# Kernel tuning notes

Hardware: AMD Instinct MI355X
Metric: run time of the kernel (lower is better)

## Reference

```python
import jax, jax.numpy as jnp
import numpy as np

N = 50000      # graph nodes
E = 800000     # edges
R = 8          # relations
D = 128        # entity_dim == relation_dim == n_hidden
L = 2          # gnn layers
NE = 150000    # entity vocab
NEG_SLOPE = 0.01


def setup_inputs() -> dict:
    key = jax.random.key(0)
    ks = jax.random.split(key, 9)
    return {
        "node_ids": jax.random.randint(ks[0], (N,), 0, NE),
        "relation_ids": jax.random.randint(ks[1], (E,), 0, R),
        "src": jax.random.randint(ks[2], (E,), 0, N),
        "dst": jax.random.randint(ks[3], (E,), 0, N),
        "entity_table": jax.random.normal(ks[4], (NE, D), dtype=jnp.float32) * 0.1,
        "relation_table": jax.random.normal(ks[5], (R, D), dtype=jnp.float32) * 0.1,
        "relation_W": jax.random.normal(ks[6], (R, D, D), dtype=jnp.float32) * 0.1,
        "res_fc_W": jax.random.normal(ks[7], (L, D, D), dtype=jnp.float32) * 0.1,
        "res_fc2_W": jax.random.normal(ks[8], (L, D, D), dtype=jnp.float32) * 0.1,
    }


def _kgat_layer(h, efeat, rel, src, dst, relation_W, W1, W2):
    # project every node by every relation weight: (N, R, D)
    proj = jnp.einsum('nd,rde->nre', h, relation_W)
    t_r = proj[src, rel]            # (E, D)  W_r h_src
    h_r = proj[dst, rel]            # (E, D)  W_r h_dst
    # att = (W_r h_t)^T tanh(W_r h_dst + e_r)
    att = jnp.sum(t_r * jnp.tanh(h_r + efeat), axis=1)  # (E,)
    # edge softmax over incoming edges of each dst node
    m = jax.ops.segment_max(att, dst, num_segments=N)
    ex = jnp.exp(att - m[dst])
    s = jax.ops.segment_sum(ex, dst, num_segments=N)
    a = ex / s[dst]                 # (E,)
    # message = a * h_src, scatter-sum to dst
    h_nb = jax.ops.segment_sum(h[src] * a[:, None], dst, num_segments=N)  # (N, D)
    out = (jax.nn.leaky_relu((h + h_nb) @ W1.T, NEG_SLOPE)
           + jax.nn.leaky_relu((h * h_nb) @ W2.T, NEG_SLOPE))
    return h_nb, out


def reference(node_ids, relation_ids, src, dst, entity_table, relation_table,
              relation_W, res_fc_W, res_fc2_W):
    h = entity_table[node_ids]           # (N, D)
    efeat = relation_table[relation_ids]  # (E, D)
    cache = [h]
    for i in range(L):
        h, out = _kgat_layer(h, efeat, relation_ids, src, dst,
                             relation_W, res_fc_W[i], res_fc2_W[i])
        cache.append(out)
    return jnp.concatenate(cache, axis=1)  # (N, D*(L+1))
```

## Files before the change

### kernel.cpp

```cpp
#include <hip/hip_runtime.h>
#include <math.h>

#define DDIM 128
#define RREL 8

typedef _Float16 f16;
typedef __attribute__((ext_vector_type(2))) _Float16 h2;
typedef __attribute__((ext_vector_type(8))) _Float16 f16x8;
typedef __attribute__((ext_vector_type(4))) float f32x4;

static __device__ __forceinline__ unsigned short f2h(float f) {
    union { _Float16 h; unsigned short s; } c; c.h = (_Float16)f; return c.s;
}
static __device__ __forceinline__ h2 u2h(unsigned u) {
    union { unsigned u; h2 h; } c; c.u = u; return c.h;
}
static __device__ __forceinline__ unsigned h2u(h2 h) {
    union { unsigned u; h2 h; } c; c.h = h; return c.u;
}
static __device__ __forceinline__ float lrelu(float x) {
    return x > 0.0f ? x : 0.01f * x;
}
static __device__ __forceinline__ float tanh_fast(float x) {
    return 1.0f - 2.0f / (__expf(2.0f * x) + 1.0f);
}

__global__ __launch_bounds__(256) void prep_weights(const float* __restrict__ relW,
                                                    const float* __restrict__ fcW,
                                                    const float* __restrict__ fc2W,
                                                    unsigned short* __restrict__ Wt,
                                                    unsigned short* __restrict__ Wb1,
                                                    unsigned short* __restrict__ Wb2) {
    int i = blockIdx.x * 256 + threadIdx.x;
    const int NT = RREL * DDIM * DDIM;
    const int NF = 2 * DDIM * DDIM;
    if (i < NT) {
        int r = i >> 14;
        int d = (i >> 7) & 127;
        int e = i & 127;
        Wt[(r << 14) + (e << 7) + d] = f2h(relW[i]);
    } else if (i < NT + NF) {
        int j = i - NT;
        Wb1[j] = f2h(fcW[j]);
    } else if (i < NT + 2 * NF) {
        int j = i - NT - NF;
        Wb2[j] = f2h(fc2W[j]);
    }
}

__global__ __launch_bounds__(256) void gather_h0(const int* __restrict__ node_ids,
                                                 const float* __restrict__ etab,
                                                 unsigned short* __restrict__ hb0,
                                                 float* __restrict__ out, int N) {
    int i = blockIdx.x * 256 + threadIdx.x;
    if (i >= N * 32) return;
    int n = i >> 5;
    int c4 = (i & 31) * 4;
    float4 v = *(const float4*)(etab + (size_t)node_ids[n] * DDIM + c4);
    *(float4*)(out + (size_t)n * 384 + c4) = v;
    unsigned lo = (unsigned)f2h(v.x) | ((unsigned)f2h(v.y) << 16);
    unsigned hi = (unsigned)f2h(v.z) | ((unsigned)f2h(v.w) << 16);
    *(uint2*)(hb0 + (size_t)n * DDIM + c4) = make_uint2(lo, hi);
}

__global__ __launch_bounds__(256) void hist_k(const int* __restrict__ dst,
                                              int* __restrict__ counts, int E) {
    int i = blockIdx.x * 256 + threadIdx.x;
    if (i < E) atomicAdd(counts + dst[i], 1);
}

__global__ __launch_bounds__(256) void scan_a(const int* __restrict__ counts,
                                              int* __restrict__ tmp,
                                              int* __restrict__ part, int N) {
    __shared__ int sh[256];
    int i = blockIdx.x * 256 + threadIdx.x;
    int v = (i < N) ? counts[i] : 0;
    sh[threadIdx.x] = v;
    __syncthreads();
    #pragma unroll
    for (int o = 1; o < 256; o <<= 1) {
        int t = (threadIdx.x >= o) ? sh[threadIdx.x - o] : 0;
        __syncthreads();
        sh[threadIdx.x] += t;
        __syncthreads();
    }
    if (i < N) tmp[i] = sh[threadIdx.x];
    if (threadIdx.x == 255) part[blockIdx.x] = sh[255];
}

__global__ __launch_bounds__(256) void scan_b(int* __restrict__ part, int nb) {
    __shared__ int sh[256];
    int v = (threadIdx.x < nb) ? part[threadIdx.x] : 0;
    sh[threadIdx.x] = v;
    __syncthreads();
    #pragma unroll
    for (int o = 1; o < 256; o <<= 1) {
        int t = (threadIdx.x >= o) ? sh[threadIdx.x - o] : 0;
        __syncthreads();
        sh[threadIdx.x] += t;
        __syncthreads();
    }
    if (threadIdx.x < nb) part[threadIdx.x] = sh[threadIdx.x] - v;
}

__global__ __launch_bounds__(256) void scan_c(const int* __restrict__ counts,
                                              const int* __restrict__ tmp,
                                              const int* __restrict__ part,
                                              int* __restrict__ row_ptr,
                                              int* __restrict__ woff, int N) {
    int i = blockIdx.x * 256 + threadIdx.x;
    if (i >= N) return;
    int incl = tmp[i] + part[blockIdx.x];
    row_ptr[i + 1] = incl;
    woff[i] = incl - counts[i];
    if (i == 0) row_ptr[0] = 0;
}

__global__ __launch_bounds__(256) void scatter_k(const int* __restrict__ src,
                                                 const int* __restrict__ rel,
                                                 const int* __restrict__ dst,
                                                 int* __restrict__ woff,
                                                 int2* __restrict__ epack, int E) {
    int i = blockIdx.x * 256 + threadIdx.x;
    if (i >= E) return;
    int p = atomicAdd(woff + dst[i], 1);
    epack[p] = make_int2(src[i], rel[i]);
}

__global__ __launch_bounds__(256) void proj_gemm(const unsigned short* __restrict__ hb,
                                                 const unsigned short* __restrict__ Wt,
                                                 unsigned short* __restrict__ proj, int N) {
    __shared__ __align__(16) unsigned short As[128][136];
    __shared__ __align__(16) unsigned short Bs[128][136];
    int tid = threadIdx.x;
    int row0 = blockIdx.x * 128;
    int colbase = blockIdx.y * 128;

    #pragma unroll
    for (int j = 0; j < 8; ++j) {
        int idx = j * 256 + tid;
        int row = idx >> 4;
        int c8 = (idx & 15) * 8;
        int grow = row0 + row;
        uint4 v = make_uint4(0, 0, 0, 0);
        if (grow < N) v = *(const uint4*)(hb + (size_t)grow * DDIM + c8);
        *(uint4*)(&As[row][c8]) = v;
    }
    #pragma unroll
    for (int j = 0; j < 8; ++j) {
        int idx = j * 256 + tid;
        int row = idx >> 4;
        int c8 = (idx & 15) * 8;
        *(uint4*)(&Bs[row][c8]) = *(const uint4*)(Wt + ((size_t)(colbase + row) << 7) + c8);
    }
    __syncthreads();

    int wave = tid >> 6, lane = tid & 63;
    int wr = wave >> 1, wc = wave & 1;
    int m = lane & 15, quad = lane >> 4;

    f32x4 acc[4][4];
    #pragma unroll
    for (int mt = 0; mt < 4; ++mt)
        #pragma unroll
        for (int nt = 0; nt < 4; ++nt) acc[mt][nt] = (f32x4){0.f, 0.f, 0.f, 0.f};

    #pragma unroll
    for (int kk = 0; kk < 4; ++kk) {
        f16x8 af[4], bfr[4];
        #pragma unroll
        for (int i = 0; i < 4; ++i)
            af[i] = *(const f16x8*)(&As[wr * 64 + i * 16 + m][kk * 32 + quad * 8]);
        #pragma unroll
        for (int i = 0; i < 4; ++i)
            bfr[i] = *(const f16x8*)(&Bs[wc * 64 + i * 16 + m][kk * 32 + quad * 8]);
        #pragma unroll
        for (int mt = 0; mt < 4; ++mt)
            #pragma unroll
            for (int nt = 0; nt < 4; ++nt)
                acc[mt][nt] = __builtin_amdgcn_mfma_f32_16x16x32_f16(af[mt], bfr[nt], acc[mt][nt], 0, 0, 0);
    }

    #pragma unroll
    for (int mt = 0; mt < 4; ++mt) {
        #pragma unroll
        for (int nt = 0; nt < 4; ++nt) {
            #pragma unroll
            for (int q = 0; q < 4; ++q) {
                int row = row0 + wr * 64 + mt * 16 + quad * 4 + q;
                int col = colbase + wc * 64 + nt * 16 + m;
                if (row < N)
                    proj[(size_t)row * 1024 + col] = f2h(acc[mt][nt][q]);
            }
        }
    }
}

__global__ __launch_bounds__(256) void fused_agg(const unsigned short* __restrict__ proj,
                                                 const unsigned short* __restrict__ hb,
                                                 const float* __restrict__ rtab,
                                                 const int* __restrict__ row_ptr,
                                                 const int2* __restrict__ epack,
                                                 unsigned short* __restrict__ hbn, int N) {
    __shared__ __align__(16) unsigned th2[4][RREL][68];
    int wv = threadIdx.x >> 6, lane = threadIdx.x & 63;
    int n = blockIdx.x * 4 + wv;
    if (n >= N) return;
    int g  = lane >> 3;
    int gp = lane & 7;
    int d0 = lane * 2;
    int dbase = gp * 16;

    #pragma unroll
    for (int r = 0; r < RREL; ++r) {
        unsigned pw = *(const unsigned*)(proj + (size_t)n * 1024 + r * 128 + d0);
        h2 pv = u2h(pw);
        float2 rv = *(const float2*)(rtab + r * DDIM + d0);
        h2 t;
        t.x = (_Float16)tanh_fast((float)pv.x + rv.x);
        t.y = (_Float16)tanh_fast((float)pv.y + rv.y);
        th2[wv][r][lane] = h2u(t);
    }

    int beg = row_ptr[n], end = row_ptr[n + 1];
    float s = 0.f;
    h2 a[8];
    #pragma unroll
    for (int i = 0; i < 8; ++i) a[i] = u2h(0u);

    for (int base = beg; base < end; base += 8) {
        int eidx = base + g;
        bool act = eidx < end;
        int2 ep = act ? epack[eidx] : make_int2(0, 0);
        int sr = ep.x, rr = ep.y;
        const unsigned short* pp = proj + (size_t)sr * 1024 + rr * 128 + dbase;
        const unsigned short* hp = hb + (size_t)sr * DDIM + dbase;
        uint4 pv0 = *(const uint4*)(pp);
        uint4 pv1 = *(const uint4*)(pp + 8);
        uint4 hv0 = *(const uint4*)(hp);
        uint4 hv1 = *(const uint4*)(hp + 8);
        const unsigned* tp = &th2[wv][rr][gp * 8];
        uint4 t0 = *(const uint4*)(tp);
        uint4 t1 = *(const uint4*)(tp + 4);

        h2 vs = u2h(pv0.x) * u2h(t0.x);
        vs += u2h(pv0.y) * u2h(t0.y);
        vs += u2h(pv0.z) * u2h(t0.z);
        vs += u2h(pv0.w) * u2h(t0.w);
        vs += u2h(pv1.x) * u2h(t1.x);
        vs += u2h(pv1.y) * u2h(t1.y);
        vs += u2h(pv1.z) * u2h(t1.z);
        vs += u2h(pv1.w) * u2h(t1.w);
        float v = (float)vs.x + (float)vs.y;
        v += __shfl_xor(v, 1, 64);
        v += __shfl_xor(v, 2, 64);
        v += __shfl_xor(v, 4, 64);

        float p = act ? __expf(fminf(v, 10.f)) : 0.f;
        s += p;
        h2 ph;
        ph.x = (_Float16)p;
        ph.y = ph.x;
        a[0] += ph * u2h(hv0.x);
        a[1] += ph * u2h(hv0.y);
        a[2] += ph * u2h(hv0.z);
        a[3] += ph * u2h(hv0.w);
        a[4] += ph * u2h(hv1.x);
        a[5] += ph * u2h(hv1.y);
        a[6] += ph * u2h(hv1.z);
        a[7] += ph * u2h(hv1.w);
    }

    #pragma unroll
    for (int st = 8; st < 64; st <<= 1) {
        s += __shfl_xor(s, st, 64);
        #pragma unroll
        for (int i = 0; i < 8; ++i) {
            unsigned t = (unsigned)__shfl_xor((int)h2u(a[i]), st, 64);
            a[i] += u2h(t);
        }
    }

    float inv = (end > beg) ? 1.0f / s : 0.0f;

    if (g == 0) {
        unsigned pk[8];
        #pragma unroll
        for (int i = 0; i < 8; ++i) {
            float lo = (float)a[i].x * inv;
            float hi = (float)a[i].y * inv;
            h2 o;
            o.x = (_Float16)lo;
            o.y = (_Float16)hi;
            pk[i] = h2u(o);
        }
        unsigned short* bp = hbn + (size_t)n * DDIM + gp * 16;
        *(uint4*)(bp)     = make_uint4(pk[0], pk[1], pk[2], pk[3]);
        *(uint4*)(bp + 8) = make_uint4(pk[4], pk[5], pk[6], pk[7]);
    }
}

__global__ __launch_bounds__(256) void out_gemm(const unsigned short* __restrict__ hb,
                                                const unsigned short* __restrict__ hbn,
                                                const unsigned short* __restrict__ W1,
                                                const unsigned short* __restrict__ W2,
                                                float* __restrict__ out,
                                                int colbase, int N) {
    __shared__ __align__(16) unsigned short As[64][136];
    __shared__ __align__(16) unsigned short Bs[128][136];
    int tid = threadIdx.x;
    int row0 = blockIdx.x * 64;
    int wave = tid >> 6, lane = tid & 63;
    int m = lane & 15, quad = lane >> 4;

    f32x4 acc[2][8];
    #pragma unroll
    for (int p = 0; p < 2; ++p)
        #pragma unroll
        for (int t = 0; t < 8; ++t) acc[p][t] = (f32x4){0.f, 0.f, 0.f, 0.f};

    #pragma unroll
    for (int p = 0; p < 2; ++p) {
        #pragma unroll
        for (int j = 0; j < 4; ++j) {
            int idx = j * 256 + tid;
            int row = idx >> 4;
            int c8 = (idx & 15) * 8;
            int grow = row0 + row;
            unsigned pk[4] = {0, 0, 0, 0};
            if (grow < N) {
                uint4 hv = *(const uint4*)(hb + (size_t)grow * DDIM + c8);
                uint4 nv = *(const uint4*)(hbn + (size_t)grow * DDIM + c8);
                unsigned hw[4] = {hv.x, hv.y, hv.z, hv.w};
                unsigned nw[4] = {nv.x, nv.y, nv.z, nv.w};
                #pragma unroll
                for (int jj = 0; jj < 4; ++jj) {
                    h2 hh = u2h(hw[jj]), nn = u2h(nw[jj]);
                    h2 r = p ? (h2)(hh * nn) : (h2)(hh + nn);
                    pk[jj] = h2u(r);
                }
            }
            *(uint4*)(&As[row][c8]) = make_uint4(pk[0], pk[1], pk[2], pk[3]);
        }
        const unsigned short* W = p ? W2 : W1;
        #pragma unroll
        for (int j = 0; j < 8; ++j) {
            int idx = j * 256 + tid;
            int brow = idx >> 4;
            int c8 = (idx & 15) * 8;
            *(uint4*)(&Bs[brow][c8]) = *(const uint4*)(W + ((size_t)brow << 7) + c8);
        }
        __syncthreads();

        #pragma unroll
        for (int kk = 0; kk < 4; ++kk) {
            f16x8 av = *(const f16x8*)(&As[wave * 16 + m][kk * 32 + quad * 8]);
            #pragma unroll
            for (int t = 0; t < 8; ++t) {
                f16x8 b = *(const f16x8*)(&Bs[t * 16 + m][kk * 32 + quad * 8]);
                acc[p][t] = __builtin_amdgcn_mfma_f32_16x16x32_f16(av, b, acc[p][t], 0, 0, 0);
            }
        }
        __syncthreads();
    }

    #pragma unroll
    for (int t = 0; t < 8; ++t) {
        #pragma unroll
        for (int q = 0; q < 4; ++q) {
            int row = row0 + wave * 16 + quad * 4 + q;
            int col = t * 16 + m;
            if (row < N)
                out[(size_t)row * 384 + colbase + col] =
                    lrelu(acc[0][t][q]) + lrelu(acc[1][t][q]);
        }
    }
}

extern "C" void kernel_launch(void* const* d_in, const int* in_sizes, int n_in,
                              void* d_out, int out_size, void* d_ws, size_t ws_size,
                              hipStream_t stream) {
    const int* node_ids = (const int*)d_in[0];
    const int* rel_ids  = (const int*)d_in[1];
    const int* src      = (const int*)d_in[2];
    const int* dst      = (const int*)d_in[3];
    const float* etab   = (const float*)d_in[4];
    const float* rtab   = (const float*)d_in[5];
    const float* relW   = (const float*)d_in[6];
    const float* fcW    = (const float*)d_in[7];
    const float* fc2W   = (const float*)d_in[8];
    float* out = (float*)d_out;

    const int N = in_sizes[0];
    const int E = in_sizes[1];
    const int NB = (N + 255) / 256;

    char* ws = (char*)d_ws;
    size_t off = 0;
    auto alloc = [&](size_t bytes) -> char* {
        char* p = ws + off;
        off = (off + bytes + 255) & ~(size_t)255;
        return p;
    };
    unsigned short* hb[3];
    hb[0] = (unsigned short*)alloc((size_t)N * DDIM * 2);
    hb[1] = (unsigned short*)alloc((size_t)N * DDIM * 2);
    hb[2] = (unsigned short*)alloc((size_t)N * DDIM * 2);
    unsigned short* Wt  = (unsigned short*)alloc((size_t)RREL * DDIM * DDIM * 2);
    unsigned short* Wb1 = (unsigned short*)alloc((size_t)2 * DDIM * DDIM * 2);
    unsigned short* Wb2 = (unsigned short*)alloc((size_t)2 * DDIM * DDIM * 2);
    unsigned short* proj = (unsigned short*)alloc((size_t)N * RREL * DDIM * 2);
    int*  counts  = (int*)alloc((size_t)N * 4);
    int*  tmp     = (int*)alloc((size_t)N * 4);
    int*  part    = (int*)alloc((size_t)NB * 4);
    int*  row_ptr = (int*)alloc((size_t)(N + 1) * 4);
    int*  woff    = (int*)alloc((size_t)N * 4);
    int2* epack   = (int2*)alloc((size_t)E * 8);

    const int NW = RREL * DDIM * DDIM + 4 * DDIM * DDIM;
    hipLaunchKernelGGL(prep_weights, dim3((NW + 255) / 256), dim3(256), 0, stream,
                       relW, fcW, fc2W, Wt, Wb1, Wb2);
    hipLaunchKernelGGL(gather_h0, dim3((N * 32 + 255) / 256), dim3(256), 0, stream,
                       node_ids, etab, hb[0], out, N);

    hipMemsetAsync(counts, 0, (size_t)N * 4, stream);
    hipLaunchKernelGGL(hist_k, dim3((E + 255) / 256), dim3(256), 0, stream, dst, counts, E);
    hipLaunchKernelGGL(scan_a, dim3(NB), dim3(256), 0, stream, counts, tmp, part, N);
    hipLaunchKernelGGL(scan_b, dim3(1), dim3(256), 0, stream, part, NB);
    hipLaunchKernelGGL(scan_c, dim3(NB), dim3(256), 0, stream, counts, tmp, part, row_ptr, woff, N);
    hipLaunchKernelGGL(scatter_k, dim3((E + 255) / 256), dim3(256), 0, stream,
                       src, rel_ids, dst, woff, epack, E);

    for (int l = 0; l < 2; ++l) {
        hipLaunchKernelGGL(proj_gemm, dim3((N + 127) / 128, 8), dim3(256), 0, stream,
                           hb[l], Wt, proj, N);
        hipLaunchKernelGGL(fused_agg, dim3((N + 3) / 4), dim3(256), 0, stream,
                           proj, hb[l], rtab, row_ptr, epack, hb[l + 1], N);
        hipLaunchKernelGGL(out_gemm, dim3((N + 63) / 64), dim3(256), 0, stream,
                           hb[l], hb[l + 1], Wb1 + (size_t)l * DDIM * DDIM, Wb2 + (size_t)l * DDIM * DDIM,
                           out, (l + 1) * DDIM, N);
    }
}
```

Baseline: 507.7 us.

## Fold relation projection into per-dst query vector to avoid gathering projected sources

Rewrites the attention score (W_r h_src)·tanh(W_r h_dst + e_r) as h_src·(W_r^T tanh(W_r h_dst + e_r)). The GEMM kernel now computes the tanh term in registers, stages it in shared memory and runs a second MFMA against W_r to produce a per-destination query for each relation. The edge loop then reads only the 128-wide h_src row it already needed for messages, instead of also gathering a random 256-byte slice of the N×8×128 projection. The cost is a second GEMM per tile and an extra transposed weight copy, plus rounding the intermediate tanh to fp16.

Measured after the change: 512.0 us. Within noise of the previous version (+0.8%).

```diff
diff --git a/kernel.cpp b/kernel.cpp
--- a/kernel.cpp
+++ b/kernel.cpp
@@ -29,16 +29,20 @@
                                                     const float* __restrict__ fcW,
                                                     const float* __restrict__ fc2W,
                                                     unsigned short* __restrict__ Wt,
+                                                    unsigned short* __restrict__ Wq,
                                                     unsigned short* __restrict__ Wb1,
                                                     unsigned short* __restrict__ Wb2) {
     int i = blockIdx.x * 256 + threadIdx.x;
     const int NT = RREL * DDIM * DDIM;
     const int NF = 2 * DDIM * DDIM;
     if (i < NT) {
+        float w = relW[i];
         int r = i >> 14;
         int d = (i >> 7) & 127;
         int e = i & 127;
-        Wt[(r << 14) + (e << 7) + d] = f2h(relW[i]);
+        unsigned short h = f2h(w);
+        Wt[(r << 14) + (e << 7) + d] = h;
+        Wq[i] = h;
     } else if (i < NT + NF) {
         int j = i - NT;
         Wb1[j] = f2h(fcW[j]);
@@ -127,14 +131,16 @@
     epack[p] = make_int2(src[i], rel[i]);
 }
 
-__global__ __launch_bounds__(256) void proj_gemm(const unsigned short* __restrict__ hb,
-                                                 const unsigned short* __restrict__ Wt,
-                                                 unsigned short* __restrict__ proj, int N) {
+__global__ __launch_bounds__(256) void prq_gemm(const unsigned short* __restrict__ hb,
+                                                const unsigned short* __restrict__ Wt,
+                                                const unsigned short* __restrict__ Wq,
+                                                const float* __restrict__ rtab,
+                                                unsigned short* __restrict__ qout, int N) {
     __shared__ __align__(16) unsigned short As[128][136];
     __shared__ __align__(16) unsigned short Bs[128][136];
     int tid = threadIdx.x;
     int row0 = blockIdx.x * 128;
-    int colbase = blockIdx.y * 128;
+    int r = blockIdx.y;
 
     #pragma unroll
     for (int j = 0; j < 8; ++j) {
@@ -145,21 +151,62 @@
         uint4 v = make_uint4(0, 0, 0, 0);
         if (grow < N) v = *(const uint4*)(hb + (size_t)grow * DDIM + c8);
         *(uint4*)(&As[row][c8]) = v;
+        *(uint4*)(&Bs[row][c8]) = *(const uint4*)(Wt + (r << 14) + (row << 7) + c8);
+    }
+    __syncthreads();
+
+    int wave = tid >> 6, lane = tid & 63;
+    int wr = wave >> 1, wc = wave & 1;
+    int m = lane & 15, quad = lane >> 4;
+
+    f32x4 acc[4][4];
+    #pragma unroll
+    for (int mt = 0; mt < 4; ++mt)
+        #pragma unroll
+        for (int nt = 0; nt < 4; ++nt) acc[mt][nt] = (f32x4){0.f, 0.f, 0.f, 0.f};
+
+    #pragma unroll
+    for (int kk = 0; kk < 4; ++kk) {
+        f16x8 af[4], bfr[4];
+        #pragma unroll
+        for (int i = 0; i < 4; ++i)
+            af[i] = *(const f16x8*)(&As[wr * 64 + i * 16 + m][kk * 32 + quad * 8]);
+        #pragma unroll
+        for (int i = 0; i < 4; ++i)
+            bfr[i] = *(const f16x8*)(&Bs[wc * 64 + i * 16 + m][kk * 32 + quad * 8]);
+        #pragma unroll
+        for (int mt = 0; mt < 4; ++mt)
+            #pragma unroll
+            for (int nt = 0; nt < 4; ++nt)
+                acc[mt][nt] = __builtin_amdgcn_mfma_f32_16x16x32_f16(af[mt], bfr[nt], acc[mt][nt], 0, 0, 0);
+    }
+    __syncthreads();
+
+    float rv[4];
+    #pragma unroll
+    for (int nt = 0; nt < 4; ++nt)
+        rv[nt] = rtab[r * DDIM + wc * 64 + nt * 16 + m];
+    #pragma unroll
+    for (int mt = 0; mt < 4; ++mt) {
+        #pragma unroll
+        for (int nt = 0; nt < 4; ++nt) {
+            #pragma unroll
+            for (int q = 0; q < 4; ++q) {
+                int row = wr * 64 + mt * 16 + quad * 4 + q;
+                int col = wc * 64 + nt * 16 + m;
+                As[row][col] = f2h(tanh_fast(acc[mt][nt][q] + rv[nt]));
+            }
+        }
     }
     #pragma unroll
     for (int j = 0; j < 8; ++j) {
         int idx = j * 256 + tid;
         int row = idx >> 4;
         int c8 = (idx & 15) * 8;
-        *(uint4*)(&Bs[row][c8]) = *(const uint4*)(Wt + ((size_t)(colbase + row) << 7) + c8);
+        *(uint4*)(&Bs[row][c8]) = *(const uint4*)(Wq + (r << 14) + (row << 7) + c8);
     }
     __syncthreads();
 
-    int wave = tid >> 6, lane = tid & 63;
-    int wr = wave >> 1, wc = wave & 1;
-    int m = lane & 15, quad = lane >> 4;
-
-    f32x4 acc[4][4];
     #pragma unroll
     for (int mt = 0; mt < 4; ++mt)
         #pragma unroll
@@ -188,39 +235,30 @@
             #pragma unroll
             for (int q = 0; q < 4; ++q) {
                 int row = row0 + wr * 64 + mt * 16 + quad * 4 + q;
-                int col = colbase + wc * 64 + nt * 16 + m;
+                int col = wc * 64 + nt * 16 + m;
                 if (row < N)
-                    proj[(size_t)row * 1024 + col] = f2h(acc[mt][nt][q]);
+                    qout[(size_t)row * 1024 + (r << 7) + col] = f2h(acc[mt][nt][q]);
             }
         }
     }
 }
 
-__global__ __launch_bounds__(256) void fused_agg(const unsigned short* __restrict__ proj,
+__global__ __launch_bounds__(256) void fused_agg(const unsigned short* __restrict__ qt,
                                                  const unsigned short* __restrict__ hb,
-                                                 const float* __restrict__ rtab,
                                                  const int* __restrict__ row_ptr,
                                                  const int2* __restrict__ epack,
                                                  unsigned short* __restrict__ hbn, int N) {
-    __shared__ __align__(16) unsigned th2[4][RREL][68];
+    __shared__ __align__(16) unsigned q2[4][RREL][68];
     int wv = threadIdx.x >> 6, lane = threadIdx.x & 63;
     int n = blockIdx.x * 4 + wv;
     if (n >= N) return;
     int g  = lane >> 3;
     int gp = lane & 7;
-    int d0 = lane * 2;
     int dbase = gp * 16;
 
     #pragma unroll
-    for (int r = 0; r < RREL; ++r) {
-        unsigned pw = *(const unsigned*)(proj + (size_t)n * 1024 + r * 128 + d0);
-        h2 pv = u2h(pw);
-        float2 rv = *(const float2*)(rtab + r * DDIM + d0);
-        h2 t;
-        t.x = (_Float16)tanh_fast((float)pv.x + rv.x);
-        t.y = (_Float16)tanh_fast((float)pv.y + rv.y);
-        th2[wv][r][lane] = h2u(t);
-    }
+    for (int r = 0; r < RREL; ++r)
+        q2[wv][r][lane] = *(const unsigned*)(qt + (size_t)n * 1024 + r * 128 + lane * 2);
 
     int beg = row_ptr[n], end = row_ptr[n + 1];
     float s = 0.f;
@@ -233,24 +271,21 @@
         bool act = eidx < end;
         int2 ep = act ? epack[eidx] : make_int2(0, 0);
         int sr = ep.x, rr = ep.y;
-        const unsigned short* pp = proj + (size_t)sr * 1024 + rr * 128 + dbase;
         const unsigned short* hp = hb + (size_t)sr * DDIM + dbase;
-        uint4 pv0 = *(const uint4*)(pp);
-        uint4 pv1 = *(const uint4*)(pp + 8);
         uint4 hv0 = *(const uint4*)(hp);
         uint4 hv1 = *(const uint4*)(hp + 8);
-        const unsigned* tp = &th2[wv][rr][gp * 8];
+        const unsigned* tp = &q2[wv][rr][gp * 8];
         uint4 t0 = *(const uint4*)(tp);
         uint4 t1 = *(const uint4*)(tp + 4);
 
-        h2 vs = u2h(pv0.x) * u2h(t0.x);
-        vs += u2h(pv0.y) * u2h(t0.y);
-        vs += u2h(pv0.z) * u2h(t0.z);
-        vs += u2h(pv0.w) * u2h(t0.w);
-        vs += u2h(pv1.x) * u2h(t1.x);
-        vs += u2h(pv1.y) * u2h(t1.y);
-        vs += u2h(pv1.z) * u2h(t1.z);
-        vs += u2h(pv1.w) * u2h(t1.w);
+        h2 vs = u2h(hv0.x) * u2h(t0.x);
+        vs += u2h(hv0.y) * u2h(t0.y);
+        vs += u2h(hv0.z) * u2h(t0.z);
+        vs += u2h(hv0.w) * u2h(t0.w);
+        vs += u2h(hv1.x) * u2h(t1.x);
+        vs += u2h(hv1.y) * u2h(t1.y);
+        vs += u2h(hv1.z) * u2h(t1.z);
+        vs += u2h(hv1.w) * u2h(t1.w);
         float v = (float)vs.x + (float)vs.y;
         v += __shfl_xor(v, 1, 64);
         v += __shfl_xor(v, 2, 64);
@@ -407,9 +442,10 @@
     hb[1] = (unsigned short*)alloc((size_t)N * DDIM * 2);
     hb[2] = (unsigned short*)alloc((size_t)N * DDIM * 2);
     unsigned short* Wt  = (unsigned short*)alloc((size_t)RREL * DDIM * DDIM * 2);
+    unsigned short* Wq  = (unsigned short*)alloc((size_t)RREL * DDIM * DDIM * 2);
     unsigned short* Wb1 = (unsigned short*)alloc((size_t)2 * DDIM * DDIM * 2);
     unsigned short* Wb2 = (unsigned short*)alloc((size_t)2 * DDIM * DDIM * 2);
-    unsigned short* proj = (unsigned short*)alloc((size_t)N * RREL * DDIM * 2);
+    unsigned short* qt  = (unsigned short*)alloc((size_t)N * RREL * DDIM * 2);
     int*  counts  = (int*)alloc((size_t)N * 4);
     int*  tmp     = (int*)alloc((size_t)N * 4);
     int*  part    = (int*)alloc((size_t)NB * 4);
@@ -419,7 +455,7 @@
 
     const int NW = RREL * DDIM * DDIM + 4 * DDIM * DDIM;
     hipLaunchKernelGGL(prep_weights, dim3((NW + 255) / 256), dim3(256), 0, stream,
-                       relW, fcW, fc2W, Wt, Wb1, Wb2);
+                       relW, fcW, fc2W, Wt, Wq, Wb1, Wb2);
     hipLaunchKernelGGL(gather_h0, dim3((N * 32 + 255) / 256), dim3(256), 0, stream,
                        node_ids, etab, hb[0], out, N);
 
@@ -432,10 +468,10 @@
                        src, rel_ids, dst, woff, epack, E);
 
     for (int l = 0; l < 2; ++l) {
-        hipLaunchKernelGGL(proj_gemm, dim3((N + 127) / 128, 8), dim3(256), 0, stream,
-                           hb[l], Wt, proj, N);
+        hipLaunchKernelGGL(prq_gemm, dim3((N + 127) / 128, 8), dim3(256), 0, stream,
+                           hb[l], Wt, Wq, rtab, qt, N);
         hipLaunchKernelGGL(fused_agg, dim3((N + 3) / 4), dim3(256), 0, stream,
-                           proj, hb[l], rtab, row_ptr, epack, hb[l + 1], N);
+                           qt, hb[l], row_ptr, epack, hb[l + 1], N);
         hipLaunchKernelGGL(out_gemm, dim3((N + 63) / 64), dim3(256), 0, stream,
                            hb[l], hb[l + 1], Wb1 + (size_t)l * DDIM * DDIM, Wb2 + (size_t)l * DDIM * DDIM,
                            out, (l + 1) * DDIM, N);
```
